# Performance work log

Measured on AMD Instinct MI355X. Metric: run time of the kernel, lower is better.

Reference implementation:

```python
import jax, jax.numpy as jnp
import numpy as np

VOCAB, BLOCK, C, H, L = 65, 60, 384, 6, 6
HS = C // H  # 64
EPS = 1e-5


def _ln(x, g, b):
    mu = jnp.mean(x, axis=-1, keepdims=True)
    var = jnp.mean(jnp.square(x - mu), axis=-1, keepdims=True)
    return (x - mu) * jax.lax.rsqrt(var + EPS) * g + b


def setup_inputs() -> dict:
    key = jax.random.key(0)
    ks = jax.random.split(key, 16)
    std = 0.02
    B, T = 2048, 60
    inp = {
        'context': jax.random.randint(ks[0], (B, T), 0, VOCAB),
        'tok_emb': std * jax.random.normal(ks[1], (VOCAB, C), jnp.float32),
        'pos_emb': std * jax.random.normal(ks[2], (BLOCK, C), jnp.float32),
        # per-head projections stacked: [L, H, C, HS]
        'wq': std * jax.random.normal(ks[3], (L, H, C, HS), jnp.float32),
        'wk': std * jax.random.normal(ks[4], (L, H, C, HS), jnp.float32),
        'wv': std * jax.random.normal(ks[5], (L, H, C, HS), jnp.float32),
        'wo': std * jax.random.normal(ks[6], (L, C, C), jnp.float32),
        'bo': jnp.zeros((L, C), jnp.float32),
        'ln1_g': jnp.ones((L, C), jnp.float32),
        'ln1_b': jnp.zeros((L, C), jnp.float32),
        'ln2_g': jnp.ones((L, C), jnp.float32),
        'ln2_b': jnp.zeros((L, C), jnp.float32),
        'w1': std * jax.random.normal(ks[7], (L, C, 4 * C), jnp.float32),
        'b1': jnp.zeros((L, 4 * C), jnp.float32),
        'w2': std * jax.random.normal(ks[8], (L, 4 * C, C), jnp.float32),
        'b2': jnp.zeros((L, C), jnp.float32),
        'lnf_g': jnp.ones((C,), jnp.float32),
        'lnf_b': jnp.zeros((C,), jnp.float32),
        'lm_w': std * jax.random.normal(ks[9], (C, VOCAB), jnp.float32),
        'lm_b': jnp.zeros((VOCAB,), jnp.float32),
    }
    return inp


def _forward(context, tok_emb, pos_emb, wq, wk, wv, wo, bo,
             ln1_g, ln1_b, ln2_g, ln2_b, w1, b1, w2, b2,
             lnf_g, lnf_b, lm_w, lm_b):
    B, T = context.shape
    x = tok_emb[context] + pos_emb[:T]  # [B,T,C]
    causal = jnp.tril(jnp.ones((T, T), bool))
    neg_inf = jnp.finfo(x.dtype).min

    def block(x, p):
        (wq_l, wk_l, wv_l, wo_l, bo_l, g1, b1n, g2, b2n, w1_l, bb1, w2_l, bb2) = p
        h = _ln(x, g1, b1n)
        q = jnp.einsum('btc,hcd->bhtd', h, wq_l)
        k = jnp.einsum('btc,hcd->bhtd', h, wk_l)
        v = jnp.einsum('btc,hcd->bhtd', h, wv_l)
        scores = jnp.einsum('bhtd,bhsd->bhts', q, k) * (HS ** -0.5)
        scores = jnp.where(causal, scores, neg_inf)
        probs = jax.nn.softmax(scores, axis=-1)
        o = jnp.einsum('bhts,bhsd->bhtd', probs, v)
        o = o.transpose(0, 2, 1, 3).reshape(B, T, C)  # concat heads
        x = x + o @ wo_l + bo_l
        h = _ln(x, g2, b2n)
        x = x + jax.nn.relu(h @ w1_l + bb1) @ w2_l + bb2
        return x, None

    params = (wq, wk, wv, wo, bo, ln1_g, ln1_b, ln2_g, ln2_b, w1, b1, w2, b2)
    x, _ = jax.lax.scan(block, x, params)
    x = _ln(x, lnf_g, lnf_b)
    return x @ lm_w + lm_b  # [B,T,VOCAB]


def reference(context, tok_emb, pos_emb, wq, wk, wv, wo, bo,
              ln1_g, ln1_b, ln2_g, ln2_b, w1, b1, w2, b2,
              lnf_g, lnf_b, lm_w, lm_b):
    return _forward(context, tok_emb, pos_emb, wq, wk, wv, wo, bo,
                    ln1_g, ln1_b, ln2_g, ln2_b, w1, b1, w2, b2,
                    lnf_g, lnf_b, lm_w, lm_b)
```

## Files before the change

kernel.cpp:

```cpp
#include <hip/hip_runtime.h>


#define B_  2048
#define T_  60
#define C_  384
#define H_  6
#define HS_ 64
#define L_  6
#define FF_ 1536
#define V_  65

typedef unsigned int  u32;
typedef unsigned short u16;
typedef short bf16x8 __attribute__((ext_vector_type(8)));
typedef float f32x4  __attribute__((ext_vector_type(4)));

__device__ __forceinline__ float bf2f(u32 u) {
  return __uint_as_float(u << 16);
}
__device__ __forceinline__ u16 f2bf(float f) {
  u32 u = __float_as_uint(f);
  u = u + 0x7FFFu + ((u >> 16) & 1u);
  return (u16)(u >> 16);
}

typedef const __attribute__((address_space(1))) unsigned int gas_u32;
typedef __attribute__((address_space(3))) unsigned int las_u32;
__device__ __forceinline__ void gload16(const u16* g, u16* l) {
  __builtin_amdgcn_global_load_lds((gas_u32*)g, (las_u32*)l, 16, 0, 0);
}

__global__ void tconv_k(const float* __restrict__ src, u16* __restrict__ dst,
                        int K, int N, long srcStride, int nH, long sL, long sH)
{
  __shared__ float t[32][33];
  int z = blockIdx.z;
  int l = z / nH, hh = z % nH;
  const float* s = src + (long)z * srcStride;
  u16* d = dst + l * sL + hh * sH;
  int n0 = blockIdx.x * 32, k0 = blockIdx.y * 32;
  for (int yy = threadIdx.y; yy < 32; yy += 8) {
    int k = k0 + yy, n = n0 + threadIdx.x;
    t[yy][threadIdx.x] = (k < K && n < N) ? s[(long)k * N + n] : 0.f;
  }
  __syncthreads();
  for (int yy = threadIdx.y; yy < 32; yy += 8) {
    int n = n0 + yy, k = k0 + threadIdx.x;
    if (n < N && k < K) d[(long)n * K + k] = f2bf(t[threadIdx.x][yy]);
  }
}

__global__ __launch_bounds__(256) void embed_k(const int* __restrict__ ctx,
    const float* __restrict__ tok, const float* __restrict__ pos,
    float* __restrict__ x)
{
  int idx = blockIdx.x * 256 + threadIdx.x;
  int row = idx / (C_ / 4);
  int c   = (idx % (C_ / 4)) * 4;
  int t   = row % T_;
  int tk  = ctx[row];
  float4 a = *(const float4*)(tok + (long)tk * C_ + c);
  float4 p = *(const float4*)(pos + (long)t  * C_ + c);
  float4 o = make_float4(a.x + p.x, a.y + p.y, a.z + p.z, a.w + p.w);
  *(float4*)(x + (long)idx * 4) = o;
}

__global__ __launch_bounds__(256) void ln_k(const float* __restrict__ x,
    const float* __restrict__ g, const float* __restrict__ b,
    u16* __restrict__ h)
{
  int lane = threadIdx.x & 63;
  int wv   = threadIdx.x >> 6;
  long row = (long)blockIdx.x * 4 + wv;
  const float* xr = x + row * C_;
  int c0 = lane * 6;
  float v0[6];
  #pragma unroll
  for (int i = 0; i < 6; i++) v0[i] = xr[c0 + i];
  float s = 0.f, sq = 0.f;
  #pragma unroll
  for (int i = 0; i < 6; i++) { s += v0[i]; sq += v0[i] * v0[i]; }
  #pragma unroll
  for (int off = 32; off > 0; off >>= 1) {
    s  += __shfl_xor(s,  off, 64);
    sq += __shfl_xor(sq, off, 64);
  }
  float mu  = s * (1.f / C_);
  float var = sq * (1.f / C_) - mu * mu;
  float rs  = rsqrtf(var + 1e-5f);
  u16* hr = h + row * C_;
  #pragma unroll
  for (int i = 0; i < 6; i++) {
    float hv = (v0[i] - mu) * rs * g[c0 + i] + b[c0 + i];
    hr[c0 + i] = f2bf(hv);
  }
}

template<int RELU, int RES, int OBF>
__global__ __launch_bounds__(512) void gemm256p(const u16* __restrict__ A,
    const u16* __restrict__ Wt, const float* __restrict__ bias,
    const float* __restrict__ resid, void* __restrict__ outp,
    int N, int K, int mT, int nT)
{
  __shared__ __align__(16) u16 As[3][256][4][8];
  __shared__ __align__(16) u16 Bs[3][128][4][8];
  int tid = threadIdx.x;
  int bid = blockIdx.x;
  int mtile, ntile;
  if ((mT & 7) == 0) {
    int xcd = bid & 7, loc = bid >> 3;
    int q = loc / nT;
    mtile = xcd * (mT >> 3) + q;
    ntile = loc - q * nT;
  } else {
    int q = bid / nT;
    mtile = q;
    ntile = bid - q * nT;
  }
  long mBase = (long)mtile * 256;
  int  nBase = ntile * 128;
  int lane = tid & 63, wv = tid >> 6;
  int l15 = lane & 15, l4 = lane >> 4;
  int wr = wv >> 1, wc = wv & 1;
  int srow = tid >> 2;
  int seg  = (tid & 3) ^ ((tid >> 4) & 3);
  const u16* aL0 = A  + (mBase + srow) * (long)K + seg * 8;
  const u16* aL1 = aL0 + (long)128 * K;
  const u16* bL  = Wt + ((long)nBase + srow) * K + seg * 8;
  int wvOff = wv << 9;
  u16* a0 = &As[0][0][0][0];
  u16* a1 = &As[1][0][0][0];
  u16* a2 = &As[2][0][0][0];
  u16* b0 = &Bs[0][0][0][0];
  u16* b1 = &Bs[1][0][0][0];
  u16* b2 = &Bs[2][0][0][0];
  int swR  = l4 ^ (l15 >> 2);
  int aOff = ((wr * 64 + l15) * 4 + swR) * 8;
  int bOff = ((wc * 64 + l15) * 4 + swR) * 8;

  f32x4 acc[4][4];
  #pragma unroll
  for (int i = 0; i < 4; i++)
    #pragma unroll
    for (int j = 0; j < 4; j++)
      acc[i][j] = (f32x4){0.f, 0.f, 0.f, 0.f};

  const int NT = K >> 5;
  gload16(aL0,      a0 + wvOff);
  gload16(aL1,      a0 + 4096 + wvOff);
  gload16(bL,       b0 + wvOff);
  gload16(aL0 + 32, a1 + wvOff);
  gload16(aL1 + 32, a1 + 4096 + wvOff);
  gload16(bL  + 32, b1 + wvOff);

  for (int t = 0; t < NT; ++t) {
    if (t + 1 < NT)
      asm volatile("s_waitcnt vmcnt(3) lgkmcnt(0)\n\ts_barrier" ::: "memory");
    else
      asm volatile("s_waitcnt vmcnt(0) lgkmcnt(0)\n\ts_barrier" ::: "memory");
    int k2 = (t + 2) << 5;
    if (k2 < K) {
      gload16(aL0 + k2, a2 + wvOff);
      gload16(aL1 + k2, a2 + 4096 + wvOff);
      gload16(bL  + k2, b2 + wvOff);
    }
    bf16x8 af[4], bfr[4];
    #pragma unroll
    for (int i = 0; i < 4; i++)
      af[i] = *(const bf16x8*)(a0 + aOff + i * 512);
    #pragma unroll
    for (int j = 0; j < 4; j++)
      bfr[j] = *(const bf16x8*)(b0 + bOff + j * 512);
    #pragma unroll
    for (int i = 0; i < 4; i++)
      #pragma unroll
      for (int j = 0; j < 4; j++)
        acc[i][j] = __builtin_amdgcn_mfma_f32_16x16x32_bf16(
            af[i], bfr[j], acc[i][j], 0, 0, 0);
    u16* tA = a0; a0 = a1; a1 = a2; a2 = tA;
    u16* tB = b0; b0 = b1; b1 = b2; b2 = tB;
  }

  #pragma unroll
  for (int i = 0; i < 4; i++) {
    #pragma unroll
    for (int j = 0; j < 4; j++) {
      int n = nBase + wc * 64 + j * 16 + l15;
      float bv = bias ? bias[n] : 0.f;
      #pragma unroll
      for (int r = 0; r < 4; r++) {
        long row = mBase + wr * 64 + i * 16 + l4 * 4 + r;
        float vv = acc[i][j][r] + bv;
        if (RELU) vv = fmaxf(vv, 0.f);
        if (RES)  vv += resid[row * N + n];
        if (OBF) ((u16*)outp)[row * N + n] = f2bf(vv);
        else     ((float*)outp)[row * N + n] = vv;
      }
    }
  }
}

template<int OBF>
__global__ __launch_bounds__(256) void gemm_head(const u16* __restrict__ A,
    const u16* __restrict__ Wt, const float* __restrict__ bias,
    void* __restrict__ outp, int N, int K)
{
  __shared__ __align__(16) u16 As[128][4][8];
  __shared__ __align__(16) u16 Bs[64][4][8];
  int tid  = threadIdx.x;
  int nt   = blockIdx.x;
  int nBase = nt * 64;
  long mBase = (long)blockIdx.y * 128;
  int lane = tid & 63, wv = tid >> 6;
  int l15 = lane & 15, l4 = lane >> 4;
  int sseg = tid & 3;
  int srow = tid >> 2;
  int swW = sseg ^ ((srow >> 2) & 3);
  int swR = l4 ^ (l15 >> 2);
  const u16* a0p = A + (mBase + srow) * K + sseg * 8;
  const u16* a1p = a0p + (long)64 * K;
  bool colOK = (nBase + srow) < N;
  const u16* bp  = Wt + (long)(nBase + srow) * K + sseg * 8;

  f32x4 acc[2][4];
  #pragma unroll
  for (int i = 0; i < 2; i++)
    #pragma unroll
    for (int j = 0; j < 4; j++)
      acc[i][j] = (f32x4){0.f, 0.f, 0.f, 0.f};

  for (int k0 = 0; k0 < K; k0 += 32) {
    uint4 av0 = *(const uint4*)(a0p + k0);
    uint4 av1 = *(const uint4*)(a1p + k0);
    uint4 bv  = colOK ? *(const uint4*)(bp + k0) : make_uint4(0, 0, 0, 0);
    *(uint4*)&As[srow][swW][0]      = av0;
    *(uint4*)&As[srow + 64][swW][0] = av1;
    *(uint4*)&Bs[srow][swW][0]      = bv;
    __syncthreads();
    bf16x8 af[2], bfr[4];
    af[0] = *(const bf16x8*)&As[wv * 32 + l15][swR][0];
    af[1] = *(const bf16x8*)&As[wv * 32 + 16 + l15][swR][0];
    #pragma unroll
    for (int j = 0; j < 4; j++)
      bfr[j] = *(const bf16x8*)&Bs[j * 16 + l15][swR][0];
    #pragma unroll
    for (int i = 0; i < 2; i++)
      #pragma unroll
      for (int j = 0; j < 4; j++)
        acc[i][j] = __builtin_amdgcn_mfma_f32_16x16x32_bf16(
            af[i], bfr[j], acc[i][j], 0, 0, 0);
    __syncthreads();
  }

  #pragma unroll
  for (int i = 0; i < 2; i++) {
    #pragma unroll
    for (int j = 0; j < 4; j++) {
      int n = nBase + j * 16 + l15;
      if (n < N) {
        #pragma unroll
        for (int r = 0; r < 4; r++) {
          long row = mBase + wv * 32 + i * 16 + l4 * 4 + r;
          float vv = acc[i][j][r];
          if (bias) vv += bias[n];
          if (OBF) ((u16*)outp)[row * N + n] = f2bf(vv);
          else     ((float*)outp)[row * N + n] = vv;
        }
      }
    }
  }
}

__global__ __launch_bounds__(256) void attn_k(const u16* __restrict__ qkv,
    u16* __restrict__ ao)
{
  __shared__ __align__(16) u16 qs[64][72];
  __shared__ __align__(16) u16 ks[64][72];
  __shared__ __align__(16) u16 vT[64][72];
  __shared__ __align__(16) u16 ps[64][72];
  int tid = threadIdx.x;
  int bb = blockIdx.x / H_;
  int hh = blockIdx.x % H_;
  const u16* base = qkv + ((long)bb * T_) * 1152 + hh * HS_;

  for (int i = tid; i < 576; i += 256)
    ((uint4*)vT)[i] = make_uint4(0, 0, 0, 0);
  __syncthreads();

  for (int i = tid; i < 480; i += 256) {
    int t = i >> 3, d0 = (i & 7) << 3;
    const u16* rp = base + (long)t * 1152;
    *(uint4*)&qs[t][d0] = *(const uint4*)(rp + d0);
    *(uint4*)&ks[t][d0] = *(const uint4*)(rp + 384 + d0);
    uint4 rv = *(const uint4*)(rp + 768 + d0);
    u16 vv[8] = {(u16)(rv.x & 0xffffu), (u16)(rv.x >> 16),
                 (u16)(rv.y & 0xffffu), (u16)(rv.y >> 16),
                 (u16)(rv.z & 0xffffu), (u16)(rv.z >> 16),
                 (u16)(rv.w & 0xffffu), (u16)(rv.w >> 16)};
    #pragma unroll
    for (int m = 0; m < 8; m++) vT[d0 + m][t] = vv[m];
  }
  __syncthreads();

  int lane = tid & 63, wv = tid >> 6;
  int l15 = lane & 15, quad = lane >> 4;

  bf16x8 aq0 = *(const bf16x8*)&qs[wv * 16 + l15][quad * 8];
  bf16x8 aq1 = *(const bf16x8*)&qs[wv * 16 + l15][32 + quad * 8];
  f32x4 s[4];
  #pragma unroll
  for (int jt = 0; jt < 4; jt++) {
    bf16x8 b0 = *(const bf16x8*)&ks[jt * 16 + l15][quad * 8];
    bf16x8 b1 = *(const bf16x8*)&ks[jt * 16 + l15][32 + quad * 8];
    f32x4 a2 = (f32x4){0.f, 0.f, 0.f, 0.f};
    a2 = __builtin_amdgcn_mfma_f32_16x16x32_bf16(aq0, b0, a2, 0, 0, 0);
    a2 = __builtin_amdgcn_mfma_f32_16x16x32_bf16(aq1, b1, a2, 0, 0, 0);
    s[jt] = a2;
  }

  int rbase = wv * 16 + quad * 4;
  #pragma unroll
  for (int r = 0; r < 4; r++) {
    int row = rbase + r;
    float v0[4];
    #pragma unroll
    for (int jt = 0; jt < 4; jt++) {
      int col = jt * 16 + l15;
      float sv = s[jt][r] * 0.125f;
      v0[jt] = (col <= row) ? sv : -1e30f;
    }
    float m = fmaxf(fmaxf(v0[0], v0[1]), fmaxf(v0[2], v0[3]));
    #pragma unroll
    for (int off = 1; off < 16; off <<= 1) m = fmaxf(m, __shfl_xor(m, off, 64));
    float sum = 0.f;
    #pragma unroll
    for (int jt = 0; jt < 4; jt++) { v0[jt] = __expf(v0[jt] - m); sum += v0[jt]; }
    #pragma unroll
    for (int off = 1; off < 16; off <<= 1) sum += __shfl_xor(sum, off, 64);
    float inv = 1.f / sum;
    #pragma unroll
    for (int jt = 0; jt < 4; jt++)
      ps[row][jt * 16 + l15] = f2bf(v0[jt] * inv);
  }
  __syncthreads();

  bf16x8 ap0 = *(const bf16x8*)&ps[wv * 16 + l15][quad * 8];
  bf16x8 ap1 = *(const bf16x8*)&ps[wv * 16 + l15][32 + quad * 8];
  long obase = ((long)bb * T_) * C_ + hh * HS_;
  #pragma unroll
  for (int dt = 0; dt < 4; dt++) {
    bf16x8 b0 = *(const bf16x8*)&vT[dt * 16 + l15][quad * 8];
    bf16x8 b1 = *(const bf16x8*)&vT[dt * 16 + l15][32 + quad * 8];
    f32x4 a2 = (f32x4){0.f, 0.f, 0.f, 0.f};
    a2 = __builtin_amdgcn_mfma_f32_16x16x32_bf16(ap0, b0, a2, 0, 0, 0);
    a2 = __builtin_amdgcn_mfma_f32_16x16x32_bf16(ap1, b1, a2, 0, 0, 0);
    #pragma unroll
    for (int r = 0; r < 4; r++) {
      int row = rbase + r;
      if (row < T_)
        ao[obase + (long)row * C_ + dt * 16 + l15] = f2bf(a2[r]);
    }
  }
}

extern "C" void kernel_launch(void* const* d_in, const int* in_sizes, int n_in,
                              void* d_out, int out_size, void* d_ws, size_t ws_size,
                              hipStream_t stream)
{
  const int*   ctx  = (const int*)  d_in[0];
  const float* tok  = (const float*)d_in[1];
  const float* pos  = (const float*)d_in[2];
  const float* wq   = (const float*)d_in[3];
  const float* wk   = (const float*)d_in[4];
  const float* wv   = (const float*)d_in[5];
  const float* wo   = (const float*)d_in[6];
  const float* bo   = (const float*)d_in[7];
  const float* ln1g = (const float*)d_in[8];
  const float* ln1b = (const float*)d_in[9];
  const float* ln2g = (const float*)d_in[10];
  const float* ln2b = (const float*)d_in[11];
  const float* w1   = (const float*)d_in[12];
  const float* b1   = (const float*)d_in[13];
  const float* w2   = (const float*)d_in[14];
  const float* b2   = (const float*)d_in[15];
  const float* lnfg = (const float*)d_in[16];
  const float* lnfb = (const float*)d_in[17];
  const float* lmw  = (const float*)d_in[18];
  const float* lmb  = (const float*)d_in[19];
  float* out = (float*)d_out;

  const long nQKV = (long)L_ * H_ * C_ * HS_;
  const long nWO  = (long)L_ * C_ * C_;
  const long nW1  = (long)L_ * C_ * FF_;
  const long nLM  = (long)C_ * V_;
  u16* wqkvT = (u16*)d_ws;
  u16* woT = wqkvT + 3 * nQKV;
  u16* w1T = woT + nWO;
  u16* w2T = w1T + nW1;
  u16* lmT = w2T + nW1;
  const size_t wbytes = (size_t)(nQKV * 3 + nWO + nW1 * 2 + nLM) * 2;

  int chunkB = 32;
  {
    const int cand[] = {2048, 1024, 512, 256, 128, 64, 32};
    for (int i = 0; i < 7; i++) {
      size_t U = (size_t)cand[i] * T_ * C_ * 2;
      if (wbytes + 7 * U <= ws_size) { chunkB = cand[i]; break; }
    }
  }
  const long BTc = (long)chunkB * T_;
  char* wsb = (char*)d_ws + wbytes;
  const size_t U = (size_t)BTc * C_ * 2;
  float* x    = (float*)wsb;
  u16*   h    = (u16*)(wsb + 2 * U);
  char*  reg  = wsb + 3 * U;
  u16* qkvb = (u16*)reg;
  u16* ab   = (u16*)(reg + 3 * U);
  u16* fb   = (u16*)reg;

  {
    dim3 tb(32, 8);
    const long sL = 1152L * 384, sH = 64L * 384, sec = 384L * 384;
    tconv_k<<<dim3(2, 12, L_ * H_), tb, 0, stream>>>(wq, wqkvT,
        C_, HS_, (long)C_ * HS_, H_, sL, sH);
    tconv_k<<<dim3(2, 12, L_ * H_), tb, 0, stream>>>(wk, wqkvT + sec,
        C_, HS_, (long)C_ * HS_, H_, sL, sH);
    tconv_k<<<dim3(2, 12, L_ * H_), tb, 0, stream>>>(wv, wqkvT + 2 * sec,
        C_, HS_, (long)C_ * HS_, H_, sL, sH);
    tconv_k<<<dim3(12, 12, L_), tb, 0, stream>>>(wo, woT,
        C_, C_, (long)C_ * C_, 1, (long)C_ * C_, 0);
    tconv_k<<<dim3(48, 12, L_), tb, 0, stream>>>(w1, w1T,
        C_, FF_, (long)C_ * FF_, 1, (long)C_ * FF_, 0);
    tconv_k<<<dim3(12, 48, L_), tb, 0, stream>>>(w2, w2T,
        FF_, C_, (long)FF_ * C_, 1, (long)FF_ * C_, 0);
    tconv_k<<<dim3(3, 12, 1), tb, 0, stream>>>(lmw, lmT,
        C_, V_, (long)C_ * V_, 1, 0, 0);
  }

  const long qkvL = 1152L * 384;
  const long woL  = (long)C_ * C_;
  const long w1L  = (long)C_ * FF_;
  dim3 blk(256);
  dim3 blk5(512);
  dim3 gEmb((u32)(BTc * C_ / 4 / 256));
  dim3 gLN((u32)(BTc / 4));
  int mT = (int)(BTc / 256);
  dim3 gHd(2, (u32)(BTc / 128));
  dim3 gAt((u32)(chunkB * H_));

  for (int c0 = 0; c0 < B_; c0 += chunkB) {
    const long tok0 = (long)c0 * T_;
    const int* ctxc = ctx + tok0;
    float* outc = out + tok0 * V_;

    embed_k<<<gEmb, blk, 0, stream>>>(ctxc, tok, pos, x);

    for (int l = 0; l < L_; l++) {
      ln_k<<<gLN, blk, 0, stream>>>(x, ln1g + l * C_, ln1b + l * C_, h);
      gemm256p<0,0,1><<<dim3(mT * 9), blk5, 0, stream>>>(h, wqkvT + l * qkvL,
          nullptr, nullptr, qkvb, 1152, C_, mT, 9);
      attn_k<<<gAt, blk, 0, stream>>>(qkvb, ab);
      gemm256p<0,1,0><<<dim3(mT * 3), blk5, 0, stream>>>(ab, woT + l * woL,
          bo + l * C_, x, x, C_, C_, mT, 3);
      ln_k<<<gLN, blk, 0, stream>>>(x, ln2g + l * C_, ln2b + l * C_, h);
      gemm256p<1,0,1><<<dim3(mT * 12), blk5, 0, stream>>>(h, w1T + l * w1L,
          b1 + l * FF_, nullptr, fb, FF_, C_, mT, 12);
      gemm256p<0,1,0><<<dim3(mT * 3), blk5, 0, stream>>>(fb, w2T + l * w1L,
          b2 + l * C_, x, x, C_, FF_, mT, 3);
    }

    ln_k<<<gLN, blk, 0, stream>>>(x, lnfg, lnfb, h);
    gemm_head<0><<<gHd, blk, 0, stream>>>(h, lmT, lmb, outc, V_, C_);
  }
}
```

Before: 5.895 ms.

## Restructure GEMM main loop with 64-wide K tiles and interleaved MFMA/load phases

The GEMM kernel now stages 64-wide K slices with an XOR swizzle over 8 chunks, triple-buffered in one flat LDS array. Each iteration is split into four barrier-separated phases that interleave LDS fragment reads, async global-to-LDS loads for stage t+2 and MFMA groups, with sched_barrier and setprio around the MFMA groups. This halves the number of K iterations and tries to overlap memory traffic with matrix-core work more tightly. The cost is more barriers per iteration and higher LDS use per block (about 144KB), which may reduce occupancy. The minimum chunk size also rises from 32 to 64.

```diff
diff --git a/kernel.cpp b/kernel.cpp
--- a/kernel.cpp
+++ b/kernel.cpp
@@ -29,6 +29,7 @@
 __device__ __forceinline__ void gload16(const u16* g, u16* l) {
   __builtin_amdgcn_global_load_lds((gas_u32*)g, (las_u32*)l, 16, 0, 0);
 }
+#define MFMA16(a, b, c) __builtin_amdgcn_mfma_f32_16x16x32_bf16((a), (b), (c), 0, 0, 0)
 
 __global__ void tconv_k(const float* __restrict__ src, u16* __restrict__ dst,
                         int K, int N, long srcStride, int nH, long sL, long sH)
@@ -97,13 +98,12 @@
 }
 
 template<int RELU, int RES, int OBF>
-__global__ __launch_bounds__(512) void gemm256p(const u16* __restrict__ A,
+__global__ __launch_bounds__(512) void gemm8p(const u16* __restrict__ A,
     const u16* __restrict__ Wt, const float* __restrict__ bias,
     const float* __restrict__ resid, void* __restrict__ outp,
     int N, int K, int mT, int nT)
 {
-  __shared__ __align__(16) u16 As[3][256][4][8];
-  __shared__ __align__(16) u16 Bs[3][128][4][8];
+  __shared__ __align__(16) u16 lds[3 * 24576];
   int tid = threadIdx.x;
   int bid = blockIdx.x;
   int mtile, ntile;
@@ -119,24 +119,20 @@
   }
   long mBase = (long)mtile * 256;
   int  nBase = ntile * 128;
-  int lane = tid & 63, wv = tid >> 6;
+  int w = tid >> 6, lane = tid & 63;
   int l15 = lane & 15, l4 = lane >> 4;
-  int wr = wv >> 1, wc = wv & 1;
-  int srow = tid >> 2;
-  int seg  = (tid & 3) ^ ((tid >> 4) & 3);
-  const u16* aL0 = A  + (mBase + srow) * (long)K + seg * 8;
-  const u16* aL1 = aL0 + (long)128 * K;
-  const u16* bL  = Wt + ((long)nBase + srow) * K + seg * 8;
-  int wvOff = wv << 9;
-  u16* a0 = &As[0][0][0][0];
-  u16* a1 = &As[1][0][0][0];
-  u16* a2 = &As[2][0][0][0];
-  u16* b0 = &Bs[0][0][0][0];
-  u16* b1 = &Bs[1][0][0][0];
-  u16* b2 = &Bs[2][0][0][0];
-  int swR  = l4 ^ (l15 >> 2);
-  int aOff = ((wr * 64 + l15) * 4 + swR) * 8;
-  int bOff = ((wc * 64 + l15) * 4 + swR) * 8;
+  int wr = w >> 1, wc = w & 1;
+  int srow = tid >> 3;
+  int ci   = (tid & 7) ^ (srow & 7);
+  const u16* aS = A  + (mBase + srow) * (long)K + ci * 8;
+  const u16* bS = Wt + ((long)nBase + srow) * K + ci * 8;
+  const long aJ = (long)64 * K;
+  int dA = (w * 64) * 8;
+  int dB = 16384 + (w * 64) * 8;
+  int cx0 = ( l4      ^ (l15 & 7)) * 8;
+  int cx1 = ((4 + l4) ^ (l15 & 7)) * 8;
+  int aRd = (wr * 64 + l15) * 64;
+  int bRd = 16384 + (wc * 64 + l15) * 64;
 
   f32x4 acc[4][4];
   #pragma unroll
@@ -145,40 +141,92 @@
     for (int j = 0; j < 4; j++)
       acc[i][j] = (f32x4){0.f, 0.f, 0.f, 0.f};
 
-  const int NT = K >> 5;
-  gload16(aL0,      a0 + wvOff);
-  gload16(aL1,      a0 + 4096 + wvOff);
-  gload16(bL,       b0 + wvOff);
-  gload16(aL0 + 32, a1 + wvOff);
-  gload16(aL1 + 32, a1 + 4096 + wvOff);
-  gload16(bL  + 32, b1 + wvOff);
-
+  const int NT = K >> 6;
+  #pragma unroll
+  for (int j = 0; j < 4; j++) gload16(aS + j * aJ,      &lds[dA + j * 4096]);
+  #pragma unroll
+  for (int j = 0; j < 2; j++) gload16(bS + j * aJ,      &lds[dB + j * 4096]);
+  #pragma unroll
+  for (int j = 0; j < 4; j++) gload16(aS + j * aJ + 64, &lds[24576 + dA + j * 4096]);
+  #pragma unroll
+  for (int j = 0; j < 2; j++) gload16(bS + j * aJ + 64, &lds[24576 + dB + j * 4096]);
+
+  int sb = 0, s2b = 2 * 24576;
   for (int t = 0; t < NT; ++t) {
-    if (t + 1 < NT)
-      asm volatile("s_waitcnt vmcnt(3) lgkmcnt(0)\n\ts_barrier" ::: "memory");
-    else
-      asm volatile("s_waitcnt vmcnt(0) lgkmcnt(0)\n\ts_barrier" ::: "memory");
-    int k2 = (t + 2) << 5;
-    if (k2 < K) {
-      gload16(aL0 + k2, a2 + wvOff);
-      gload16(aL1 + k2, a2 + 4096 + wvOff);
-      gload16(bL  + k2, b2 + wvOff);
-    }
-    bf16x8 af[4], bfr[4];
+    if (t + 1 < NT) asm volatile("s_waitcnt vmcnt(6)" ::: "memory");
+    else            asm volatile("s_waitcnt vmcnt(0)" ::: "memory");
+    __builtin_amdgcn_s_barrier();
+    long kst = (long)(t + 2) * 64;
+    bool st = (t + 2) < NT;
+    bf16x8 a0[4], a1[4], bA, bB;
     #pragma unroll
     for (int i = 0; i < 4; i++)
-      af[i] = *(const bf16x8*)(a0 + aOff + i * 512);
-    #pragma unroll
-    for (int j = 0; j < 4; j++)
-      bfr[j] = *(const bf16x8*)(b0 + bOff + j * 512);
+      a0[i] = *(const bf16x8*)&lds[sb + aRd + i * 1024 + cx0];
+    bA = *(const bf16x8*)&lds[sb + bRd + cx0];
+    bB = *(const bf16x8*)&lds[sb + bRd + 1024 + cx0];
+    if (st) {
+      gload16(aS + kst,      &lds[s2b + dA]);
+      gload16(aS + aJ + kst, &lds[s2b + dA + 4096]);
+    }
+    __builtin_amdgcn_sched_barrier(0);
+    __builtin_amdgcn_s_barrier();
+    __builtin_amdgcn_s_setprio(1);
+    #pragma unroll
+    for (int i = 0; i < 4; i++) acc[i][0] = MFMA16(a0[i], bA, acc[i][0]);
+    #pragma unroll
+    for (int i = 0; i < 4; i++) acc[i][1] = MFMA16(a0[i], bB, acc[i][1]);
+    __builtin_amdgcn_s_setprio(0);
+    __builtin_amdgcn_sched_barrier(0);
+    __builtin_amdgcn_s_barrier();
+    bA = *(const bf16x8*)&lds[sb + bRd + 2048 + cx0];
+    bB = *(const bf16x8*)&lds[sb + bRd + 3072 + cx0];
+    if (st) {
+      gload16(aS + 2 * aJ + kst, &lds[s2b + dA + 8192]);
+      gload16(aS + 3 * aJ + kst, &lds[s2b + dA + 12288]);
+    }
+    __builtin_amdgcn_sched_barrier(0);
+    __builtin_amdgcn_s_barrier();
+    __builtin_amdgcn_s_setprio(1);
+    #pragma unroll
+    for (int i = 0; i < 4; i++) acc[i][2] = MFMA16(a0[i], bA, acc[i][2]);
+    #pragma unroll
+    for (int i = 0; i < 4; i++) acc[i][3] = MFMA16(a0[i], bB, acc[i][3]);
+    __builtin_amdgcn_s_setprio(0);
+    __builtin_amdgcn_sched_barrier(0);
+    __builtin_amdgcn_s_barrier();
     #pragma unroll
     for (int i = 0; i < 4; i++)
-      #pragma unroll
-      for (int j = 0; j < 4; j++)
-        acc[i][j] = __builtin_amdgcn_mfma_f32_16x16x32_bf16(
-            af[i], bfr[j], acc[i][j], 0, 0, 0);
-    u16* tA = a0; a0 = a1; a1 = a2; a2 = tA;
-    u16* tB = b0; b0 = b1; b1 = b2; b2 = tB;
+      a1[i] = *(const bf16x8*)&lds[sb + aRd + i * 1024 + cx1];
+    bA = *(const bf16x8*)&lds[sb + bRd + cx1];
+    bB = *(const bf16x8*)&lds[sb + bRd + 1024 + cx1];
+    if (st) {
+      gload16(bS + kst,      &lds[s2b + dB]);
+      gload16(bS + aJ + kst, &lds[s2b + dB + 4096]);
+    }
+    __builtin_amdgcn_sched_barrier(0);
+    __builtin_amdgcn_s_barrier();
+    __builtin_amdgcn_s_setprio(1);
+    #pragma unroll
+    for (int i = 0; i < 4; i++) acc[i][0] = MFMA16(a1[i], bA, acc[i][0]);
+    #pragma unroll
+    for (int i = 0; i < 4; i++) acc[i][1] = MFMA16(a1[i], bB, acc[i][1]);
+    __builtin_amdgcn_s_setprio(0);
+    __builtin_amdgcn_sched_barrier(0);
+    __builtin_amdgcn_s_barrier();
+    bA = *(const bf16x8*)&lds[sb + bRd + 2048 + cx1];
+    bB = *(const bf16x8*)&lds[sb + bRd + 3072 + cx1];
+    __builtin_amdgcn_sched_barrier(0);
+    __builtin_amdgcn_s_barrier();
+    __builtin_amdgcn_s_setprio(1);
+    #pragma unroll
+    for (int i = 0; i < 4; i++) acc[i][2] = MFMA16(a1[i], bA, acc[i][2]);
+    #pragma unroll
+    for (int i = 0; i < 4; i++) acc[i][3] = MFMA16(a1[i], bB, acc[i][3]);
+    __builtin_amdgcn_s_setprio(0);
+    __builtin_amdgcn_sched_barrier(0);
+    __builtin_amdgcn_s_barrier();
+    sb  = (sb  == 2 * 24576) ? 0 : sb  + 24576;
+    s2b = (s2b == 2 * 24576) ? 0 : s2b + 24576;
   }
 
   #pragma unroll
@@ -400,10 +448,10 @@
   u16* lmT = w2T + nW1;
   const size_t wbytes = (size_t)(nQKV * 3 + nWO + nW1 * 2 + nLM) * 2;
 
-  int chunkB = 32;
+  int chunkB = 64;
   {
-    const int cand[] = {2048, 1024, 512, 256, 128, 64, 32};
-    for (int i = 0; i < 7; i++) {
+    const int cand[] = {2048, 1024, 512, 256, 128, 64};
+    for (int i = 0; i < 6; i++) {
       size_t U = (size_t)cand[i] * T_ * C_ * 2;
       if (wbytes + 7 * U <= ws_size) { chunkB = cand[i]; break; }
     }
@@ -457,15 +505,15 @@
 
     for (int l = 0; l < L_; l++) {
       ln_k<<<gLN, blk, 0, stream>>>(x, ln1g + l * C_, ln1b + l * C_, h);
-      gemm256p<0,0,1><<<dim3(mT * 9), blk5, 0, stream>>>(h, wqkvT + l * qkvL,
+      gemm8p<0,0,1><<<dim3(mT * 9), blk5, 0, stream>>>(h, wqkvT + l * qkvL,
           nullptr, nullptr, qkvb, 1152, C_, mT, 9);
       attn_k<<<gAt, blk, 0, stream>>>(qkvb, ab);
-      gemm256p<0,1,0><<<dim3(mT * 3), blk5, 0, stream>>>(ab, woT + l * woL,
+      gemm8p<0,1,0><<<dim3(mT * 3), blk5, 0, stream>>>(ab, woT + l * woL,
           bo + l * C_, x, x, C_, C_, mT, 3);
       ln_k<<<gLN, blk, 0, stream>>>(x, ln2g + l * C_, ln2b + l * C_, h);
-      gemm256p<1,0,1><<<dim3(mT * 12), blk5, 0, stream>>>(h, w1T + l * w1L,
+      gemm8p<1,0,1><<<dim3(mT * 12), blk5, 0, stream>>>(h, w1T + l * w1L,
           b1 + l * FF_, nullptr, fb, FF_, C_, mT, 12);
-      gemm256p<0,1,0><<<dim3(mT * 3), blk5, 0, stream>>>(fb, w2T + l * w1L,
+      gemm8p<0,1,0><<<dim3(mT * 3), blk5, 0, stream>>>(fb, w2T + l * w1L,
           b2 + l * C_, x, x, C_, FF_, mT, 3);
     }
 
```

Result: slower. 6.274 ms (+6.4%).
